# Performance work log

Hardware: AMD Instinct MI355X
Metric: run time of the kernel (lower is better)

## Reference

```python
import jax, jax.numpy as jnp
import numpy as np

ALPHA = 0.2  # LeakyReLU negative slope
MASK_VAL = -9e15


def setup_inputs() -> dict:
    key = jax.random.key(0)
    k1, k2, k3, k4 = jax.random.split(key, 4)
    B, N, F_IN = 4, 2048, 256
    H, HD = 8, 32  # out_features = H*HD = 256
    x = jax.random.normal(k1, (B, N, F_IN), dtype=jnp.float32)
    adj = jax.random.randint(k2, (B, N, N), 0, 2, dtype=jnp.int32)
    W = jax.random.normal(k3, (H, F_IN, HD), dtype=jnp.float32) * (1.0 / np.sqrt(F_IN))
    a = jax.random.normal(k4, (H, 2 * HD, 1), dtype=jnp.float32) * 0.1
    return {"x": x, "adj": adj, "W": W, "a": a}


def reference(x, adj, W, a):
    # x: (B,N,F), W: (H,F,D), a: (H,2D,1)
    B, N, _ = x.shape
    H, _, D = W.shape
    Wh = jnp.einsum('bnf,hfd->bhnd', x, W)  # (B,H,N,D)
    # Split additive attention vector: cat([Wh_i, Wh_j]) @ a == Wh_i@a1 + Wh_j@a2
    a1 = a[:, :D, 0]   # (H,D)
    a2 = a[:, D:, 0]   # (H,D)
    s1 = jnp.einsum('bhnd,hd->bhn', Wh, a1)  # source scores
    s2 = jnp.einsum('bhnd,hd->bhn', Wh, a2)  # target scores
    e = jax.nn.leaky_relu(s1[:, :, :, None] + s2[:, :, None, :], negative_slope=ALPHA)  # (B,H,N,N)
    e = jnp.where(adj[:, None, :, :] == 0, MASK_VAL, e)
    attention = jax.nn.softmax(e, axis=-1)  # dropout skipped (eval mode)
    h = jnp.einsum('bhij,bhjd->bhid', attention, Wh)  # (B,H,N,D)
    h = jnp.transpose(h, (0, 2, 1, 3)).reshape(B, N, H * D)
    return jax.nn.elu(h)
```

## Files before the change

kernel.cpp:

```cpp
#include <hip/hip_runtime.h>
#include <hip/hip_bf16.h>

#define ALPHA 0.2f

typedef __attribute__((ext_vector_type(8))) short short8;
typedef __attribute__((ext_vector_type(4))) short s4;
typedef __attribute__((ext_vector_type(8))) _Float16 h8;
typedef __attribute__((ext_vector_type(2))) _Float16 h2v;
typedef __attribute__((ext_vector_type(4))) float f32x4;
typedef __attribute__((ext_vector_type(2))) short sh2;

static constexpr int B = 4, N = 2048, F = 256, H = 8, D = 32;
static constexpr int SZ_X = B * N * F, SZ_ADJ = B * N * N, SZ_W = H * F * D, SZ_A = H * 2 * D;
static const float C1 = 1.4426950408889634f;
static const float C2 = ALPHA * 1.4426950408889634f;


__device__ __forceinline__ unsigned rne16(unsigned u) {
    return u + 0x7fffu + ((u >> 16) & 1u);
}
__device__ __forceinline__ unsigned pk_rne(float a, float b) {
    return __builtin_amdgcn_perm(rne16(__float_as_uint(b)),
                                 rne16(__float_as_uint(a)), 0x07060302u);
}
__device__ __forceinline__ unsigned h2mul(unsigned a, unsigned b) {
    h2v r = __builtin_bit_cast(h2v, a) * __builtin_bit_cast(h2v, b);
    return __builtin_bit_cast(unsigned, r);
}
__device__ __forceinline__ unsigned h2max(unsigned a, unsigned b) {
    h2v r = __builtin_elementwise_max(__builtin_bit_cast(h2v, a),
                                      __builtin_bit_cast(h2v, b));
    return __builtin_bit_cast(unsigned, r);
}
__device__ __forceinline__ unsigned dup16f(float x) {
    unsigned short w = __builtin_bit_cast(unsigned short, (_Float16)x);
    return (unsigned)w | ((unsigned)w << 16);
}
__device__ __forceinline__ unsigned bits2mask(unsigned mk, unsigned mulc) {
    unsigned w = (mk & 3u) * mulc;
    sh2 s = __builtin_bit_cast(sh2, w);
    s = s >> 15;
    return __builtin_bit_cast(unsigned, s);
}

__global__ void k0_prep(const float* __restrict__ Wp, const float* __restrict__ ap,
                        unsigned short* __restrict__ WT2, float* __restrict__ AF) {
    int bid = blockIdx.x;
    int h = bid >> 5, d = bid & 31;
    int f = threadIdx.x;
    unsigned short v = (unsigned short)(rne16(__float_as_uint(Wp[(h * F + f) * D + d])) >> 16);
    WT2[(size_t)(f >> 5) * 8192 + (h * 32 + d) * 32 + (f & 31)] = v;
    if (d == 0 && f < 64) AF[h * 64 + f] = ap[h * 64 + f];
}

__global__ __launch_bounds__(256, 4) void k2_fused(const float* __restrict__ x,
                                                   const unsigned short* __restrict__ WT2,
                                                   const float* __restrict__ AF,
                                                   unsigned short* __restrict__ WHT,
                                                   float* __restrict__ S1,
                                                   _Float16* __restrict__ UH,
                                                   _Float16* __restrict__ VH,
                                                   const int* __restrict__ adj,
                                                   unsigned long long* __restrict__ bm) {
    __shared__ unsigned short XA[16 * 264];
    int bid = blockIdx.x;
    int rr = bid % 5;
    int grp = bid / 5;
    int t = threadIdx.x;

    if (rr != 4) {
        int wid = (grp * 4 + rr) * 4 + (t >> 6);
        int lane = t & 63;
        size_t base = (size_t)wid * 32;
        const int* ap2 = adj + base * 64 + lane;
        int v0[16], v1[16];
#pragma unroll
        for (int s = 0; s < 16; s++) v0[s] = ap2[(size_t)s * 64];
#pragma unroll
        for (int s = 0; s < 16; s++) v1[s] = ap2[(size_t)(16 + s) * 64];
        unsigned long long m0[16];
#pragma unroll
        for (int s = 0; s < 16; s++) m0[s] = __ballot(v0[s] != 0);
        unsigned long long m1[16];
#pragma unroll
        for (int s = 0; s < 16; s++) m1[s] = __ballot(v1[s] != 0);
        if (lane == 0) {
#pragma unroll
            for (int s = 0; s < 16; s++) bm[base + s] = m0[s];
#pragma unroll
            for (int s = 0; s < 16; s++) bm[base + 16 + s] = m1[s];
        }
        return;
    }

    int b = grp >> 7;
    int n0 = (grp & 127) * 16;
    int wave = t >> 6, lane = t & 63;
    int lm = lane & 15, lq = lane >> 4;

#pragma unroll
    for (int q = 0; q < 4; q++) {
        int idx = q * 256 + t;
        int row = idx >> 6, c16 = idx & 63;
        f32x4 v = *(const f32x4*)(x + (size_t)(b * N + n0 + row) * F + c16 * 4);
        unsigned* dst = (unsigned*)&XA[row * 264 + c16 * 4];
        dst[0] = pk_rne(v[0], v[1]);
        dst[1] = pk_rne(v[2], v[3]);
    }

    short8 bcur[4], bnext[4];
#pragma unroll
    for (int c = 0; c < 4; c++)
        bcur[c] = *(const short8*)(WT2 + (size_t)(wave * 64 + c * 16 + lm) * 32 + lq * 8);
    __syncthreads();

    f32x4 acc[4] = {};
#pragma unroll
    for (int kc = 0; kc < 8; kc++) {
        if (kc < 7) {
#pragma unroll
            for (int c = 0; c < 4; c++)
                bnext[c] = *(const short8*)(WT2 + (size_t)(kc + 1) * 8192 +
                                            (wave * 64 + c * 16 + lm) * 32 + lq * 8);
        }
        short8 afr = *(const short8*)&XA[lm * 264 + kc * 32 + lq * 8];
#pragma unroll
        for (int c = 0; c < 4; c++)
            acc[c] = __builtin_amdgcn_mfma_f32_16x16x32_bf16(afr, bcur[c], acc[c], 0, 0, 0);
#pragma unroll
        for (int c = 0; c < 4; c++) bcur[c] = bnext[c];
    }

#pragma unroll
    for (int c = 0; c < 4; c++) {
        int hd = wave * 64 + c * 16 + lm;
        unsigned short w0 = __builtin_bit_cast(unsigned short, (_Float16)acc[c][0]);
        unsigned short w1 = __builtin_bit_cast(unsigned short, (_Float16)acc[c][1]);
        unsigned short w2 = __builtin_bit_cast(unsigned short, (_Float16)acc[c][2]);
        unsigned short w3 = __builtin_bit_cast(unsigned short, (_Float16)acc[c][3]);
        uint2 pk;
        pk.x = (unsigned)w0 | ((unsigned)w1 << 16);
        pk.y = (unsigned)w2 | ((unsigned)w3 << 16);
        *(uint2*)&WHT[((size_t)b * 256 + hd) * 2048 + n0 + lq * 4] = pk;
    }
#pragma unroll
    for (int cp = 0; cp < 2; cp++) {
        int h = wave * 2 + cp;
        float a1l = AF[h * 64 + lm],      a1h = AF[h * 64 + 16 + lm];
        float a2l = AF[h * 64 + 32 + lm], a2h = AF[h * 64 + 48 + lm];
#pragma unroll
        for (int r = 0; r < 4; r++) {
            float s1p = acc[cp * 2][r] * a1l + acc[cp * 2 + 1][r] * a1h;
            float s2p = acc[cp * 2][r] * a2l + acc[cp * 2 + 1][r] * a2h;
#pragma unroll
            for (int off = 1; off <= 8; off <<= 1) {
                s1p += __shfl_xor(s1p, off);
                s2p += __shfl_xor(s2p, off);
            }
            if (lm == 0) {
                int bh = b * 8 + h, n = n0 + lq * 4 + r;
                S1[(size_t)bh * 2048 + n] = s1p;
                UH[(size_t)bh * 2048 + n] = (_Float16)exp2f(C1 * s2p);
                VH[(size_t)bh * 2048 + n] = (_Float16)exp2f(C2 * s2p);
            }
        }
    }
}

__global__ __launch_bounds__(256) void k3_attn(
    const unsigned* __restrict__ bm32,
    const unsigned short* __restrict__ WHT,
    const float* __restrict__ S1,
    const _Float16* __restrict__ UH, const _Float16* __restrict__ VH,
    float* __restrict__ out) {
    __shared__ unsigned LM[4][32 * 68];
    __shared__ unsigned short LW[4][32 * 140];
    __shared__ unsigned LU[1024], LV[1024];

    int bid = blockIdx.x;
    int bh = (bid & 7) + ((bid >> 7) << 3);
    int isup = (bid >> 3) & 15;
    int b = bh >> 3, h = bh & 7;
    int i0 = isup * 128;
    int t = threadIdx.x;
    int wave = t >> 6, lane = t & 63;
    int irow = lane & 15, quad = lane >> 4;
    int iw = i0 + wave * 32;

    {
        unsigned* lmp = LM[wave];
        const unsigned* src = bm32 + ((size_t)(b * N + iw)) * 64;
#pragma unroll 8
        for (int r = 0; r < 32; r++)
            lmp[r * 68 + lane] = src[(size_t)r * 64 + lane];
    }
    {
        ((uint4*)LU)[t] = ((const uint4*)(UH + (size_t)bh * 2048))[t];
        ((uint4*)LV)[t] = ((const uint4*)(VH + (size_t)bh * 2048))[t];
    }

    const unsigned short* wsrc = WHT + ((size_t)b * 256 + h * 32) * 2048;
    int srow = t >> 3, sseg = (t & 7) * 16;

    {
        const unsigned short* g0 = wsrc + (size_t)srow * 2048 + sseg;
        union { short8 v; s4 q[2]; } a0, c0, a1, c1;
        a0.v = *(const short8*)(g0);
        c0.v = *(const short8*)(g0 + 8);
        a1.v = *(const short8*)(g0 + 128);
        c1.v = *(const short8*)(g0 + 136);
        unsigned short* d0 = &LW[0][srow * 140 + sseg];
        *(s4*)(d0) = a0.q[0]; *(s4*)(d0 + 4) = a0.q[1];
        *(s4*)(d0 + 8) = c0.q[0]; *(s4*)(d0 + 12) = c0.q[1];
        unsigned short* d1 = &LW[1][srow * 140 + sseg];
        *(s4*)(d1) = a1.q[0]; *(s4*)(d1 + 4) = a1.q[1];
        *(s4*)(d1 + 8) = c1.q[0]; *(s4*)(d1 + 12) = c1.q[1];
    }

    float s1A = S1[(size_t)bh * 2048 + iw + irow];
    float s1B = S1[(size_t)bh * 2048 + iw + 16 + irow];
    unsigned ci2A = dup16f(exp2f((C2 - C1) * s1A));
    unsigned ci2B = dup16f(exp2f((C2 - C1) * s1B));

    union { h8 v; unsigned u[4]; } ones;
    ones.u[0] = ones.u[1] = ones.u[2] = ones.u[3] = 0x3C003C00u;

    const unsigned MUL = 0x40008000u;

    f32x4 aA0 = {0,0,0,0}, aA1 = {0,0,0,0}, aAL = {0,0,0,0};
    f32x4 aB0 = {0,0,0,0}, aB1 = {0,0,0,0}, aBL = {0,0,0,0};
    __syncthreads();

    for (int g = 0; g < 8; g++) {
        union { short8 v; s4 q[2]; } pa0, pc0, pa1, pc1;
        if (g < 7) {
            const unsigned short* g0 = wsrc + (size_t)srow * 2048 + (2 * g + 2) * 128 + sseg;
            pa0.v = *(const short8*)(g0);
            pc0.v = *(const short8*)(g0 + 8);
            pa1.v = *(const short8*)(g0 + 128);
            pc1.v = *(const short8*)(g0 + 136);
        }
        const unsigned* lmw = LM[wave];
#pragma unroll
        for (int ci = 0; ci < 2; ci++) {
            int cc = 2 * g + ci;
            const unsigned short* lwp = LW[cc & 3];
            uint4 mkqA = *(const uint4*)&lmw[irow * 68 + cc * 4];
            uint4 mkqB = *(const uint4*)&lmw[(16 + irow) * 68 + cc * 4];
            uint4 uws[4], vws[4];
            s4 bf0a[4], bf0b[4], bf1a[4], bf1b[4];
#pragma unroll
            for (int ks = 0; ks < 4; ks++) {
                int jl = ks * 32 + quad * 8;
                uws[ks] = *(const uint4*)&LU[(cc * 128 + jl) >> 1];
                vws[ks] = *(const uint4*)&LV[(cc * 128 + jl) >> 1];
                bf0a[ks] = *(const s4*)&lwp[irow * 140 + jl];
                bf0b[ks] = *(const s4*)&lwp[irow * 140 + jl + 4];
                bf1a[ks] = *(const s4*)&lwp[(16 + irow) * 140 + jl];
                bf1b[ks] = *(const s4*)&lwp[(16 + irow) * 140 + jl + 4];
            }
            unsigned mkwA[4] = { mkqA.x, mkqA.y, mkqA.z, mkqA.w };
            unsigned mkwB[4] = { mkqB.x, mkqB.y, mkqB.z, mkqB.w };
            __builtin_amdgcn_s_setprio(1);
#pragma unroll
            for (int ks = 0; ks < 4; ks++) {
                unsigned mkA = mkwA[ks] >> (quad * 8);
                unsigned mkB = mkwB[ks] >> (quad * 8);
                unsigned mA0 = bits2mask(mkA,      MUL);
                unsigned mA1 = bits2mask(mkA >> 2, MUL);
                unsigned mA2 = bits2mask(mkA >> 4, MUL);
                unsigned mA3 = bits2mask(mkA >> 6, MUL);
                unsigned mB0 = bits2mask(mkB,      MUL);
                unsigned mB1 = bits2mask(mkB >> 2, MUL);
                unsigned mB2 = bits2mask(mkB >> 4, MUL);
                unsigned mB3 = bits2mask(mkB >> 6, MUL);
                union { h8 v; unsigned u[4]; } afA, afB;
                afA.u[0] = h2max(uws[ks].x, h2mul(ci2A, vws[ks].x)) & mA0;
                afA.u[1] = h2max(uws[ks].y, h2mul(ci2A, vws[ks].y)) & mA1;
                afA.u[2] = h2max(uws[ks].z, h2mul(ci2A, vws[ks].z)) & mA2;
                afA.u[3] = h2max(uws[ks].w, h2mul(ci2A, vws[ks].w)) & mA3;
                afB.u[0] = h2max(uws[ks].x, h2mul(ci2B, vws[ks].x)) & mB0;
                afB.u[1] = h2max(uws[ks].y, h2mul(ci2B, vws[ks].y)) & mB1;
                afB.u[2] = h2max(uws[ks].z, h2mul(ci2B, vws[ks].z)) & mB2;
                afB.u[3] = h2max(uws[ks].w, h2mul(ci2B, vws[ks].w)) & mB3;
                union { short8 v; s4 q[2]; } bf0, bf1;
                bf0.q[0] = bf0a[ks]; bf0.q[1] = bf0b[ks];
                bf1.q[0] = bf1a[ks]; bf1.q[1] = bf1b[ks];
                h8 b0 = __builtin_bit_cast(h8, bf0.v);
                h8 b1 = __builtin_bit_cast(h8, bf1.v);
                aA0 = __builtin_amdgcn_mfma_f32_16x16x32_f16(afA.v, b0, aA0, 0, 0, 0);
                aA1 = __builtin_amdgcn_mfma_f32_16x16x32_f16(afA.v, b1, aA1, 0, 0, 0);
                aAL = __builtin_amdgcn_mfma_f32_16x16x32_f16(afA.v, ones.v, aAL, 0, 0, 0);
                aB0 = __builtin_amdgcn_mfma_f32_16x16x32_f16(afB.v, b0, aB0, 0, 0, 0);
                aB1 = __builtin_amdgcn_mfma_f32_16x16x32_f16(afB.v, b1, aB1, 0, 0, 0);
                aBL = __builtin_amdgcn_mfma_f32_16x16x32_f16(afB.v, ones.v, aBL, 0, 0, 0);
            }
            __builtin_amdgcn_s_setprio(0);
        }
        if (g < 7) {
            unsigned short* d0 = &LW[(2 * g + 2) & 3][srow * 140 + sseg];
            *(s4*)(d0) = pa0.q[0]; *(s4*)(d0 + 4) = pa0.q[1];
            *(s4*)(d0 + 8) = pc0.q[0]; *(s4*)(d0 + 12) = pc0.q[1];
            unsigned short* d1 = &LW[(2 * g + 3) & 3][srow * 140 + sseg];
            *(s4*)(d1) = pa1.q[0]; *(s4*)(d1 + 4) = pa1.q[1];
            *(s4*)(d1 + 8) = pc1.q[0]; *(s4*)(d1 + 12) = pc1.q[1];
        }
        __syncthreads();
    }

#pragma unroll
    for (int r = 0; r < 4; r++) {
        float lA = aAL[r], lB = aBL[r];
        float rA = 1.0f / (lA > 0.f ? lA : 1.f);
        float rB = 1.0f / (lB > 0.f ? lB : 1.f);
        float vA0 = aA0[r] * rA, vA1 = aA1[r] * rA;
        float vB0 = aB0[r] * rB, vB1 = aB1[r] * rB;
        vA0 = vA0 > 0.f ? vA0 : __expf(vA0) - 1.f;
        vA1 = vA1 > 0.f ? vA1 : __expf(vA1) - 1.f;
        vB0 = vB0 > 0.f ? vB0 : __expf(vB0) - 1.f;
        vB1 = vB1 > 0.f ? vB1 : __expf(vB1) - 1.f;
        int iA = iw + quad * 4 + r, iB = iA + 16;
        size_t rbA = (size_t)(b * N + iA) * 256 + h * 32;
        size_t rbB = (size_t)(b * N + iB) * 256 + h * 32;
        out[rbA + irow] = vA0;
        out[rbA + 16 + irow] = vA1;
        out[rbB + irow] = vB0;
        out[rbB + 16 + irow] = vB1;
    }
}

extern "C" void kernel_launch(void* const* d_in, const int* in_sizes, int n_in,
                              void* d_out, int out_size, void* d_ws, size_t ws_size,
                              hipStream_t stream) {
    const void *xP = nullptr, *adjP = nullptr, *WP = nullptr, *aP = nullptr;
    for (int i = 0; i < n_in; i++) {
        switch (in_sizes[i]) {
            case SZ_X:   xP = d_in[i]; break;
            case SZ_ADJ: adjP = d_in[i]; break;
            case SZ_W:   WP = d_in[i]; break;
            case SZ_A:   aP = d_in[i]; break;
            default: break;
        }
    }
    if (!xP || !adjP || !WP || !aP) { xP = d_in[0]; adjP = d_in[1]; WP = d_in[2]; aP = d_in[3]; }
    float* out = (float*)d_out;

    char* ws = (char*)d_ws;
    unsigned short* WT2 = (unsigned short*)(ws);
    float* AF  = (float*)(ws + 131072);
    float* S1  = (float*)(ws + 133120);
    _Float16* UH = (_Float16*)(ws + 395264);
    _Float16* VH = (_Float16*)(ws + 526336);
    unsigned short* WHT = (unsigned short*)(ws + 657408);
    unsigned long long* BM = (unsigned long long*)(ws + 4851712);

    k0_prep<<<256, 256, 0, stream>>>((const float*)WP, (const float*)aP, WT2, AF);
    k2_fused<<<2560, 256, 0, stream>>>((const float*)xP, WT2, AF, WHT, S1, UH, VH,
                                       (const int*)adjP, BM);
    k3_attn<<<512, 256, 0, stream>>>((const unsigned*)BM, WHT, S1, UH, VH, out);
}
```

Measured before the change: 139.8 us.

## Split attention key range across two wave groups with LDS reduction

Doubles the attention block to 512 threads, so two groups of four waves each process half of the key columns for the same 128 query rows. Partial accumulators are then summed through shared memory before normalisation and ELU. The W tile staging is reorganised so each half double-buffers its own column chunk. This aims to raise wave-level parallelism and latency hiding in a kernel with only 512 blocks, at the cost of an extra reduction pass, a barrier and higher register pressure under the new launch bounds.

```diff
diff --git a/kernel.cpp b/kernel.cpp
--- a/kernel.cpp
+++ b/kernel.cpp
@@ -167,7 +167,7 @@
     }
 }
 
-__global__ __launch_bounds__(256) void k3_attn(
+__global__ __launch_bounds__(512, 4) void k3_attn(
     const unsigned* __restrict__ bm32,
     const unsigned short* __restrict__ WHT,
     const float* __restrict__ S1,
@@ -184,37 +184,34 @@
     int i0 = isup * 128;
     int t = threadIdx.x;
     int wave = t >> 6, lane = t & 63;
+    int wsub = wave & 3, half = wave >> 2;
     int irow = lane & 15, quad = lane >> 4;
-    int iw = i0 + wave * 32;
-
-    {
-        unsigned* lmp = LM[wave];
+    int iw = i0 + wsub * 32;
+
+    if (half == 0) {
+        unsigned* lmp = LM[wsub];
         const unsigned* src = bm32 + ((size_t)(b * N + iw)) * 64;
 #pragma unroll 8
         for (int r = 0; r < 32; r++)
             lmp[r * 68 + lane] = src[(size_t)r * 64 + lane];
-    }
+    } else {
+        int u = t - 256;
+        ((uint4*)LU)[u] = ((const uint4*)(UH + (size_t)bh * 2048))[u];
+        ((uint4*)LV)[u] = ((const uint4*)(VH + (size_t)bh * 2048))[u];
+    }
+
+    const unsigned short* wsrc = WHT + ((size_t)b * 256 + h * 32) * 2048;
+    int srow = t >> 4, sseg = (t & 15) * 8;
+
     {
-        ((uint4*)LU)[t] = ((const uint4*)(UH + (size_t)bh * 2048))[t];
-        ((uint4*)LV)[t] = ((const uint4*)(VH + (size_t)bh * 2048))[t];
-    }
-
-    const unsigned short* wsrc = WHT + ((size_t)b * 256 + h * 32) * 2048;
-    int srow = t >> 3, sseg = (t & 7) * 16;
-
-    {
-        const unsigned short* g0 = wsrc + (size_t)srow * 2048 + sseg;
-        union { short8 v; s4 q[2]; } a0, c0, a1, c1;
-        a0.v = *(const short8*)(g0);
-        c0.v = *(const short8*)(g0 + 8);
-        a1.v = *(const short8*)(g0 + 128);
-        c1.v = *(const short8*)(g0 + 136);
+        const unsigned short* gA = wsrc + (size_t)srow * 2048 + sseg;
+        union { short8 v; s4 q[2]; } a0, a1;
+        a0.v = *(const short8*)(gA);
+        a1.v = *(const short8*)(gA + 8 * 128);
         unsigned short* d0 = &LW[0][srow * 140 + sseg];
         *(s4*)(d0) = a0.q[0]; *(s4*)(d0 + 4) = a0.q[1];
-        *(s4*)(d0 + 8) = c0.q[0]; *(s4*)(d0 + 12) = c0.q[1];
-        unsigned short* d1 = &LW[1][srow * 140 + sseg];
+        unsigned short* d1 = &LW[2][srow * 140 + sseg];
         *(s4*)(d1) = a1.q[0]; *(s4*)(d1 + 4) = a1.q[1];
-        *(s4*)(d1 + 8) = c1.q[0]; *(s4*)(d1 + 12) = c1.q[1];
     }
 
     float s1A = S1[(size_t)bh * 2048 + iw + irow];
@@ -232,38 +229,38 @@
     __syncthreads();
 
     for (int g = 0; g < 8; g++) {
-        union { short8 v; s4 q[2]; } pa0, pc0, pa1, pc1;
+        union { short8 v; s4 q[2]; } pa, pb;
         if (g < 7) {
-            const unsigned short* g0 = wsrc + (size_t)srow * 2048 + (2 * g + 2) * 128 + sseg;
-            pa0.v = *(const short8*)(g0);
-            pc0.v = *(const short8*)(g0 + 8);
-            pa1.v = *(const short8*)(g0 + 128);
-            pc1.v = *(const short8*)(g0 + 136);
-        }
-        const unsigned* lmw = LM[wave];
-#pragma unroll
-        for (int ci = 0; ci < 2; ci++) {
-            int cc = 2 * g + ci;
-            const unsigned short* lwp = LW[cc & 3];
-            uint4 mkqA = *(const uint4*)&lmw[irow * 68 + cc * 4];
-            uint4 mkqB = *(const uint4*)&lmw[(16 + irow) * 68 + cc * 4];
-            uint4 uws[4], vws[4];
-            s4 bf0a[4], bf0b[4], bf1a[4], bf1b[4];
-#pragma unroll
-            for (int ks = 0; ks < 4; ks++) {
+            const unsigned short* gA = wsrc + (size_t)srow * 2048 + (g + 1) * 128 + sseg;
+            pa.v = *(const short8*)(gA);
+            pb.v = *(const short8*)(gA + 8 * 128);
+        }
+        int cc = half * 8 + g;
+        const unsigned short* lwp = LW[half * 2 + (g & 1)];
+        const unsigned* lmw = LM[wsub];
+        uint4 mkqA = *(const uint4*)&lmw[irow * 68 + cc * 4];
+        uint4 mkqB = *(const uint4*)&lmw[(16 + irow) * 68 + cc * 4];
+        unsigned mkwA[4] = { mkqA.x, mkqA.y, mkqA.z, mkqA.w };
+        unsigned mkwB[4] = { mkqB.x, mkqB.y, mkqB.z, mkqB.w };
+#pragma unroll
+        for (int hs = 0; hs < 2; hs++) {
+            uint4 uws[2], vws[2];
+            s4 bf0a[2], bf0b[2], bf1a[2], bf1b[2];
+#pragma unroll
+            for (int k2 = 0; k2 < 2; k2++) {
+                int ks = hs * 2 + k2;
                 int jl = ks * 32 + quad * 8;
-                uws[ks] = *(const uint4*)&LU[(cc * 128 + jl) >> 1];
-                vws[ks] = *(const uint4*)&LV[(cc * 128 + jl) >> 1];
-                bf0a[ks] = *(const s4*)&lwp[irow * 140 + jl];
-                bf0b[ks] = *(const s4*)&lwp[irow * 140 + jl + 4];
-                bf1a[ks] = *(const s4*)&lwp[(16 + irow) * 140 + jl];
-                bf1b[ks] = *(const s4*)&lwp[(16 + irow) * 140 + jl + 4];
+                uws[k2] = *(const uint4*)&LU[(cc * 128 + jl) >> 1];
+                vws[k2] = *(const uint4*)&LV[(cc * 128 + jl) >> 1];
+                bf0a[k2] = *(const s4*)&lwp[irow * 140 + jl];
+                bf0b[k2] = *(const s4*)&lwp[irow * 140 + jl + 4];
+                bf1a[k2] = *(const s4*)&lwp[(16 + irow) * 140 + jl];
+                bf1b[k2] = *(const s4*)&lwp[(16 + irow) * 140 + jl + 4];
             }
-            unsigned mkwA[4] = { mkqA.x, mkqA.y, mkqA.z, mkqA.w };
-            unsigned mkwB[4] = { mkqB.x, mkqB.y, mkqB.z, mkqB.w };
             __builtin_amdgcn_s_setprio(1);
 #pragma unroll
-            for (int ks = 0; ks < 4; ks++) {
+            for (int k2 = 0; k2 < 2; k2++) {
+                int ks = hs * 2 + k2;
                 unsigned mkA = mkwA[ks] >> (quad * 8);
                 unsigned mkB = mkwB[ks] >> (quad * 8);
                 unsigned mA0 = bits2mask(mkA,      MUL);
@@ -275,17 +272,17 @@
                 unsigned mB2 = bits2mask(mkB >> 4, MUL);
                 unsigned mB3 = bits2mask(mkB >> 6, MUL);
                 union { h8 v; unsigned u[4]; } afA, afB;
-                afA.u[0] = h2max(uws[ks].x, h2mul(ci2A, vws[ks].x)) & mA0;
-                afA.u[1] = h2max(uws[ks].y, h2mul(ci2A, vws[ks].y)) & mA1;
-                afA.u[2] = h2max(uws[ks].z, h2mul(ci2A, vws[ks].z)) & mA2;
-                afA.u[3] = h2max(uws[ks].w, h2mul(ci2A, vws[ks].w)) & mA3;
-                afB.u[0] = h2max(uws[ks].x, h2mul(ci2B, vws[ks].x)) & mB0;
-                afB.u[1] = h2max(uws[ks].y, h2mul(ci2B, vws[ks].y)) & mB1;
-                afB.u[2] = h2max(uws[ks].z, h2mul(ci2B, vws[ks].z)) & mB2;
-                afB.u[3] = h2max(uws[ks].w, h2mul(ci2B, vws[ks].w)) & mB3;
+                afA.u[0] = h2max(uws[k2].x, h2mul(ci2A, vws[k2].x)) & mA0;
+                afA.u[1] = h2max(uws[k2].y, h2mul(ci2A, vws[k2].y)) & mA1;
+                afA.u[2] = h2max(uws[k2].z, h2mul(ci2A, vws[k2].z)) & mA2;
+                afA.u[3] = h2max(uws[k2].w, h2mul(ci2A, vws[k2].w)) & mA3;
+                afB.u[0] = h2max(uws[k2].x, h2mul(ci2B, vws[k2].x)) & mB0;
+                afB.u[1] = h2max(uws[k2].y, h2mul(ci2B, vws[k2].y)) & mB1;
+                afB.u[2] = h2max(uws[k2].z, h2mul(ci2B, vws[k2].z)) & mB2;
+                afB.u[3] = h2max(uws[k2].w, h2mul(ci2B, vws[k2].w)) & mB3;
                 union { short8 v; s4 q[2]; } bf0, bf1;
-                bf0.q[0] = bf0a[ks]; bf0.q[1] = bf0b[ks];
-                bf1.q[0] = bf1a[ks]; bf1.q[1] = bf1b[ks];
+                bf0.q[0] = bf0a[k2]; bf0.q[1] = bf0b[k2];
+                bf1.q[0] = bf1a[k2]; bf1.q[1] = bf1b[k2];
                 h8 b0 = __builtin_bit_cast(h8, bf0.v);
                 h8 b1 = __builtin_bit_cast(h8, bf1.v);
                 aA0 = __builtin_amdgcn_mfma_f32_16x16x32_f16(afA.v, b0, aA0, 0, 0, 0);
@@ -298,15 +295,32 @@
             __builtin_amdgcn_s_setprio(0);
         }
         if (g < 7) {
-            unsigned short* d0 = &LW[(2 * g + 2) & 3][srow * 140 + sseg];
-            *(s4*)(d0) = pa0.q[0]; *(s4*)(d0 + 4) = pa0.q[1];
-            *(s4*)(d0 + 8) = pc0.q[0]; *(s4*)(d0 + 12) = pc0.q[1];
-            unsigned short* d1 = &LW[(2 * g + 3) & 3][srow * 140 + sseg];
-            *(s4*)(d1) = pa1.q[0]; *(s4*)(d1 + 4) = pa1.q[1];
-            *(s4*)(d1 + 8) = pc1.q[0]; *(s4*)(d1 + 12) = pc1.q[1];
+            unsigned short* dA = &LW[(g + 1) & 1][srow * 140 + sseg];
+            *(s4*)(dA) = pa.q[0]; *(s4*)(dA + 4) = pa.q[1];
+            unsigned short* dB = &LW[2 + ((g + 1) & 1)][srow * 140 + sseg];
+            *(s4*)(dB) = pb.q[0]; *(s4*)(dB + 4) = pb.q[1];
         }
         __syncthreads();
     }
+
+    f32x4* sp = (f32x4*)&LW[0][0];
+    int lid = wsub * 64 + lane;
+    if (half == 1) {
+        sp[0 * 256 + lid] = aA0;
+        sp[1 * 256 + lid] = aA1;
+        sp[2 * 256 + lid] = aAL;
+        sp[3 * 256 + lid] = aB0;
+        sp[4 * 256 + lid] = aB1;
+        sp[5 * 256 + lid] = aBL;
+    }
+    __syncthreads();
+    if (half == 1) return;
+    aA0 += sp[0 * 256 + lid];
+    aA1 += sp[1 * 256 + lid];
+    aAL += sp[2 * 256 + lid];
+    aB0 += sp[3 * 256 + lid];
+    aB1 += sp[4 * 256 + lid];
+    aBL += sp[5 * 256 + lid];
 
 #pragma unroll
     for (int r = 0; r < 4; r++) {
@@ -357,5 +371,5 @@
     k0_prep<<<256, 256, 0, stream>>>((const float*)WP, (const float*)aP, WT2, AF);
     k2_fused<<<2560, 256, 0, stream>>>((const float*)xP, WT2, AF, WHT, S1, UH, VH,
                                        (const int*)adjP, BM);
-    k3_attn<<<512, 256, 0, stream>>>((const unsigned*)BM, WHT, S1, UH, VH, out);
-}
+    k3_attn<<<512, 512, 0, stream>>>((const unsigned*)BM, WHT, S1, UH, VH, out);
+}
```

After: 138.8 us. Within noise of the previous version (-0.8%).
